# Kernel optimization log

Hardware: AMD Instinct MI355X
Metric: run time of the kernel (lower is better)

The kernel has to match this reference:

```python
import jax, jax.numpy as jnp
import numpy as np

DIM = 2048
K_DIM = 2048
Q_HEADS = 16
KV_HEADS = 4
HEAD_DIM = DIM // Q_HEADS  # 128
KV_DIM = HEAD_DIM * KV_HEADS  # 512
MAX_LEN = 2048
ROPE_THETA = 10000.0
ROPE_FACTOR = 8.0


def _rope_cos_sin(seq_len):
    # Faithful to generate_sin_cos_pos_emb with is_causal=True
    d = HEAD_DIM
    seq_eff = max(seq_len, MAX_LEN)
    base_adj = (ROPE_FACTOR * seq_eff / MAX_LEN - (ROPE_FACTOR - 1.0)) ** (d / (d - 2))
    adjusted_base = ROPE_THETA * base_adj
    inv_freq = 1.0 / adjusted_base ** (np.arange(0, d, 2, dtype=np.float32) / d)
    pos = np.arange(seq_len, dtype=np.float32)  # causal: no centering
    freqs = pos[:, None] * inv_freq[None, :]            # [S, d/2]
    emb = np.concatenate([freqs, freqs], axis=-1)        # [S, d]
    return jnp.asarray(np.cos(emb), jnp.float32), jnp.asarray(np.sin(emb), jnp.float32)


def _rotate_half(x):
    x1, x2 = jnp.split(x, 2, axis=-1)
    return jnp.concatenate([-x2, x1], axis=-1)


def setup_inputs() -> dict:
    key = jax.random.key(0)
    ks = jax.random.split(key, 12)
    B, S = 1, 2048
    s_in = 1.0 / np.sqrt(DIM)
    s_k = 1.0 / np.sqrt(K_DIM)
    return {
        "query": jax.random.normal(ks[0], (B, S, DIM), jnp.float32),
        "key": jax.random.normal(ks[1], (B, S, K_DIM), jnp.float32),
        "value": jax.random.normal(ks[2], (B, S, K_DIM), jnp.float32),
        "Wq": jax.random.uniform(ks[3], (DIM, DIM), jnp.float32, -s_in, s_in),
        "bq": jax.random.uniform(ks[4], (DIM,), jnp.float32, -s_in, s_in),
        "Wk": jax.random.uniform(ks[5], (KV_DIM, K_DIM), jnp.float32, -s_k, s_k),
        "bk": jax.random.uniform(ks[6], (KV_DIM,), jnp.float32, -s_k, s_k),
        "Wv": jax.random.uniform(ks[7], (KV_DIM, K_DIM), jnp.float32, -s_k, s_k),
        "bv": jax.random.uniform(ks[8], (KV_DIM,), jnp.float32, -s_k, s_k),
        "Wo": jax.random.uniform(ks[9], (DIM, DIM), jnp.float32, -s_in, s_in),
        "bo": jax.random.uniform(ks[10], (DIM,), jnp.float32, -s_in, s_in),
    }


def reference(query, key, value, Wq, bq, Wk, bk, Wv, bv, Wo, bo):
    B, S, _ = query.shape
    scale = HEAD_DIM ** -0.5

    q = query @ Wq.T + bq                                   # [B,S,DIM]
    k = key @ Wk.T + bk                                     # [B,S,KV_DIM]
    v = value @ Wv.T + bv                                   # [B,S,KV_DIM]

    q = q.reshape(B, S, Q_HEADS, HEAD_DIM)
    k = k.reshape(B, S, KV_HEADS, HEAD_DIM)
    v = v.reshape(B, S, KV_HEADS, HEAD_DIM)

    cos, sin = _rope_cos_sin(S)                              # [S,D]
    cos = cos[None, :, None, :]
    sin = sin[None, :, None, :]
    q = q * cos + _rotate_half(q) * sin
    k = k * cos + _rotate_half(k) * sin

    # [B,H,S,D]
    q = q.transpose(0, 2, 1, 3)
    k = k.transpose(0, 2, 1, 3)
    v = v.transpose(0, 2, 1, 3)

    rep = Q_HEADS // KV_HEADS
    k = jnp.repeat(k, rep, axis=1)
    v = jnp.repeat(v, rep, axis=1)

    scores = jnp.einsum('bhqd,bhkd->bhqk', q, k) * scale
    causal = jnp.tril(jnp.ones((S, S), bool))
    scores = jnp.where(causal[None, None], scores, jnp.finfo(scores.dtype).min)
    attn = jax.nn.softmax(scores, axis=-1)
    out = jnp.einsum('bhqk,bhkd->bhqd', attn, v)             # [B,H,S,D]

    out = out.transpose(0, 2, 1, 3).reshape(B, S, DIM)
    return out @ Wo.T + bo
```

## Files before the change

### kernel.cpp

```cpp
#include <hip/hip_runtime.h>
#include <stdint.h>

typedef __attribute__((ext_vector_type(8))) short short8;
typedef __attribute__((ext_vector_type(4))) float f32x4;
typedef __attribute__((ext_vector_type(4))) unsigned short u16x4;
typedef unsigned short bf16_t;

__device__ __forceinline__ bf16_t f2bf(float f) {
  union { float f; uint32_t u; } x; x.f = f;
  uint32_t r = x.u + 0x7fffu + ((x.u >> 16) & 1u);
  return (bf16_t)(r >> 16);
}

__device__ __forceinline__ void ld_g2l_16(const bf16_t* g, bf16_t* l) {
  __builtin_amdgcn_global_load_lds(
      (const __attribute__((address_space(1))) void*)g,
      (__attribute__((address_space(3))) void*)l, 16, 0, 0);
}

__global__ void convert_all(const float* __restrict__ s0, const float* __restrict__ s1,
                            const float* __restrict__ s2, const float* __restrict__ s3,
                            const float* __restrict__ s4, const float* __restrict__ s5,
                            const float* __restrict__ s6,
                            bf16_t* __restrict__ d0, bf16_t* __restrict__ d1,
                            bf16_t* __restrict__ d2, bf16_t* __restrict__ d3,
                            bf16_t* __restrict__ d4, bf16_t* __restrict__ d5,
                            bf16_t* __restrict__ d6,
                            float* __restrict__ CS, float* __restrict__ SN) {
  int i = blockIdx.x * 256 + threadIdx.x;
  if (i < 131072) {
    int fi = i & 63, pos = i >> 6;
    float ang = (float)pos * exp2f((float)fi * -0.2076205059f);
    CS[i] = cosf(ang);
    SN[i] = sinf(ang);
  }
  const float* src; bf16_t* dst; int off;
  if (i < 5 * 1048576) {
    int t = i >> 20; off = i & 1048575;
    if (t == 0)      { src = s0; dst = d0; }
    else if (t == 1) { src = s1; dst = d1; }
    else if (t == 2) { src = s2; dst = d2; }
    else if (t == 3) { src = s3; dst = d3; }
    else             { src = s4; dst = d4; }
  } else {
    int j = i - 5 * 1048576;
    if (j < 262144) { src = s5; dst = d5; off = j; }
    else            { src = s6; dst = d6; off = j - 262144; }
  }
  f32x4 v = *(const f32x4*)(src + (size_t)off * 4);
  u16x4 o;
  o[0] = f2bf(v[0]); o[1] = f2bf(v[1]); o[2] = f2bf(v[2]); o[3] = f2bf(v[3]);
  *(u16x4*)(dst + (size_t)off * 4) = o;
}

template <int MODE>
__device__ __forceinline__ void gemm_core(
    bf16_t* __restrict__ As, bf16_t* __restrict__ Bs,
    const bf16_t* __restrict__ A, const bf16_t* __restrict__ Bm,
    const float* __restrict__ bias, void* __restrict__ Cout,
    int N, int K, int m0, int n0,
    const float* __restrict__ CS, const float* __restrict__ SN) {
  const int tid = threadIdx.x;
  const int lane = tid & 63, quad = lane >> 4, l16 = lane & 15;
  const int wv = tid >> 6;
  const int wr = wv >> 1, wc = wv & 1;

  f32x4 acc[2][4];
  const f32x4 zf = {0.f, 0.f, 0.f, 0.f};
#pragma unroll
  for (int mi = 0; mi < 2; ++mi)
#pragma unroll
    for (int ni = 0; ni < 4; ++ni) acc[mi][ni] = zf;

  const int rA = tid >> 2, cA = (tid & 3) * 8;
  const bf16_t* Ap  = A + (size_t)(m0 + rA) * K + cA;
  const bf16_t* Bp0 = Bm + (size_t)(n0 + rA) * K + cA;
  const bf16_t* Bp1 = Bm + (size_t)(n0 + 64 + rA) * K + cA;

  auto STAGE = [&](int buf, int k0) {
    ld_g2l_16(Ap + k0, As + buf * 2048 + tid * 8);
    ld_g2l_16(Bp0 + k0, Bs + buf * 4096 + tid * 8);
    ld_g2l_16(Bp1 + k0, Bs + buf * 4096 + (tid + 256) * 8);
  };

  STAGE(0, 0);
  __syncthreads();
  int buf = 0;

  for (int k0 = 0; k0 < K; k0 += 32) {
    if (k0 + 32 < K) STAGE(buf ^ 1, k0 + 32);
    const bf16_t* Ab = As + buf * 2048;
    const bf16_t* Bb = Bs + buf * 4096;
    short8 af[2], bf[4];
#pragma unroll
    for (int mi = 0; mi < 2; ++mi)
      af[mi] = *(const short8*)(&Ab[(wr * 32 + mi * 16 + l16) * 32 + quad * 8]);
#pragma unroll
    for (int ni = 0; ni < 4; ++ni)
      bf[ni] = *(const short8*)(
          &Bb[(wc * 32 + (ni & 1) * 16 + (ni >> 1) * 64 + l16) * 32 + quad * 8]);
#pragma unroll
    for (int mi = 0; mi < 2; ++mi)
#pragma unroll
      for (int ni = 0; ni < 4; ++ni)
        acc[mi][ni] = __builtin_amdgcn_mfma_f32_16x16x32_bf16(
            af[mi], bf[ni], acc[mi][ni], 0, 0, 0);
    __asm__ volatile("s_waitcnt vmcnt(0)" ::: "memory");
    __syncthreads();
    buf ^= 1;
  }

  if (MODE == 0 || MODE == 2) {
#pragma unroll
    for (int mi = 0; mi < 2; ++mi)
#pragma unroll
      for (int ni = 0; ni < 4; ++ni) {
        int n = n0 + wc * 32 + (ni & 1) * 16 + (ni >> 1) * 64 + l16;
        int mbase = m0 + wr * 32 + mi * 16 + quad * 4;
        float bv = bias[n];
#pragma unroll
        for (int r = 0; r < 4; ++r) {
          float v = acc[mi][ni][r] + bv;
          int m = mbase + r;
          if (MODE == 0) ((float*)Cout)[(size_t)m * N + n] = v;
          else           ((bf16_t*)Cout)[(size_t)n * 2048 + m] = f2bf(v);
        }
      }
  } else {
    const float scale = (MODE == 3) ? 0.12751744f : 1.0f;
    bf16_t* dst = (bf16_t*)Cout;
#pragma unroll
    for (int mi = 0; mi < 2; ++mi)
#pragma unroll
      for (int r = 0; r < 4; ++r) {
        int m = m0 + wr * 32 + mi * 16 + quad * 4 + r;
#pragma unroll
        for (int ni = 0; ni < 2; ++ni) {
          int i = wc * 32 + ni * 16 + l16;
          int n_lo = n0 + i;
          float v1 = acc[mi][ni][r] + bias[n_lo];
          float v2 = acc[mi][ni + 2][r] + bias[n_lo + 64];
          float c = CS[m * 64 + i];
          float s = SN[m * 64 + i];
          float o1 = (v1 * c - v2 * s) * scale;
          float o2 = (v2 * c + v1 * s) * scale;
          dst[(size_t)m * N + n_lo] = f2bf(o1);
          dst[(size_t)m * N + n_lo + 64] = f2bf(o2);
        }
      }
  }
}

__global__ __launch_bounds__(256) void gemm_qkv(
    const bf16_t* __restrict__ qb, const bf16_t* __restrict__ kb,
    const bf16_t* __restrict__ vb, const bf16_t* __restrict__ wqb,
    const bf16_t* __restrict__ wkb, const bf16_t* __restrict__ wvb,
    const float* __restrict__ bq, const float* __restrict__ bk,
    const float* __restrict__ bv, bf16_t* __restrict__ Qr,
    bf16_t* __restrict__ Kr, bf16_t* __restrict__ Vt,
    const float* __restrict__ CS, const float* __restrict__ SN) {
  __shared__ __align__(16) bf16_t As[2 * 64 * 32];
  __shared__ __align__(16) bf16_t Bs[2 * 128 * 32];
  int bx = blockIdx.x, m0 = blockIdx.y * 64;
  if (bx < 16)
    gemm_core<3>(As, Bs, qb, wqb, bq, Qr, 2048, 2048, m0, bx * 128, CS, SN);
  else if (bx < 20)
    gemm_core<4>(As, Bs, kb, wkb, bk, Kr, 512, 2048, m0, (bx - 16) * 128, CS, SN);
  else
    gemm_core<2>(As, Bs, vb, wvb, bv, Vt, 512, 2048, m0, (bx - 20) * 128, CS, SN);
}

__global__ __launch_bounds__(256) void gemm_o(
    const bf16_t* __restrict__ Ob, const bf16_t* __restrict__ wob,
    const float* __restrict__ bo, float* __restrict__ out) {
  __shared__ __align__(16) bf16_t As[2 * 64 * 32];
  __shared__ __align__(16) bf16_t Bs[2 * 128 * 32];
  gemm_core<0>(As, Bs, Ob, wob, bo, out, 2048, 2048,
               blockIdx.y * 64, blockIdx.x * 128, nullptr, nullptr);
}

__global__ __launch_bounds__(256, 2) void attn_fwd(
    const bf16_t* __restrict__ Qr, const bf16_t* __restrict__ Kr,
    const bf16_t* __restrict__ Vt, bf16_t* __restrict__ Oo) {
  const int h = blockIdx.y;
  const int bx = blockIdx.x;
  const int qt = (h < 8) ? (31 - bx) : bx;
  const int T = qt + 1;

  const int tid = threadIdx.x;
  const int wv = tid >> 6, lane = tid & 63, quad = lane >> 4, l16 = lane & 15;
  const int q_base = qt * 64 + wv * 16;
  const int hkv = h >> 2;
  const int qg = q_base + l16;
  const int swzE = (l16 & 7) << 3;

  __shared__ __align__(16) bf16_t Ks[2][64 * 128];
  __shared__ __align__(16) bf16_t Vs[2][128 * 64];

  short8 qf[4];
  {
    const bf16_t* qp = Qr + (size_t)qg * 2048 + h * 128 + quad * 8;
#pragma unroll
    for (int kc = 0; kc < 4; ++kc) qf[kc] = *(const short8*)(qp + kc * 32);
  }

  const f32x4 zf = {0.f, 0.f, 0.f, 0.f};
  f32x4 o[8];
#pragma unroll
  for (int di = 0; di < 8; ++di) o[di] = zf;
  float l_acc = 0.f;

  auto STAGE = [&](int buf, int t) {
    const int k0 = t * 64;
    bf16_t* KB = &Ks[buf][0];
    bf16_t* VB = &Vs[buf][0];
#pragma unroll
    for (int m = 0; m < 4; ++m) {
      int rK = wv * 16 + m * 4 + (lane >> 4);
      const bf16_t* gK = Kr + (size_t)(k0 + rK) * 512 + hkv * 128
                         + (((lane & 15) ^ ((4 * (m & 1)) | quad)) << 3);
      ld_g2l_16(gK, KB + rK * 128 + ((lane & 15) << 3));
      int rV = wv * 32 + m * 8 + (lane >> 3);
      const bf16_t* gV = Vt + (size_t)(hkv * 128 + rV) * 2048 + k0
                         + (((lane & 7) ^ ((lane >> 3) & 7)) << 3);
      ld_g2l_16(gV, VB + rV * 64 + ((lane & 7) << 3));
    }
  };

  STAGE(0, 0);
  __syncthreads();
  int buf = 0;

  for (int t = 0; t < T; ++t) {
    if (t + 1 < T) STAGE(buf ^ 1, t + 1);
    const bf16_t* KB = &Ks[buf][0];
    const bf16_t* VB = &Vs[buf][0];
    const int k0 = t * 64;

    f32x4 sacc[4];
#pragma unroll
    for (int sub = 0; sub < 4; ++sub) sacc[sub] = zf;
#pragma unroll
    for (int sub = 0; sub < 4; ++sub)
#pragma unroll
      for (int kc = 0; kc < 4; ++kc) {
        short8 kf = *(const short8*)(
            &KB[(sub * 16 + l16) * 128 + ((kc * 32 + quad * 8) ^ swzE)]);
        sacc[sub] = __builtin_amdgcn_mfma_f32_16x16x32_bf16(kf, qf[kc], sacc[sub], 0, 0, 0);
      }

    const bool dg = (k0 + 63 > q_base);
    uint32_t Dw[4][2];
#pragma unroll
    for (int sub = 0; sub < 4; ++sub) {
      float pv[4];
#pragma unroll
      for (int r = 0; r < 4; ++r) {
        float e = exp2f(sacc[sub][r]);
        if (dg) {
          int kg = k0 + sub * 16 + quad * 4 + r;
          if (kg > qg) e = 0.f;
        }
        pv[r] = e;
        l_acc += e;
      }
      asm("v_cvt_pk_bf16_f32 %0, %1, %2" : "=v"(Dw[sub][0]) : "v"(pv[0]), "v"(pv[1]));
      asm("v_cvt_pk_bf16_f32 %0, %1, %2" : "=v"(Dw[sub][1]) : "v"(pv[2]), "v"(pv[3]));
    }

    const int aA = ((((quad * 2) & 3) << 4) + l16) << 2;
    const int aB = ((((quad * 2 + 1) & 3) << 4) + l16) << 2;
    const bool losel = quad < 2;
#define BPERM(a, x) ((uint32_t)__builtin_amdgcn_ds_bpermute((a), (int)(x)))
    union { uint32_t w[4]; short8 v; } U0, U1;
    {
      uint32_t t0, t1;
      t0 = BPERM(aA, Dw[0][0]); t1 = BPERM(aA, Dw[1][0]); U0.w[0] = losel ? t0 : t1;
      t0 = BPERM(aA, Dw[0][1]); t1 = BPERM(aA, Dw[1][1]); U0.w[1] = losel ? t0 : t1;
      t0 = BPERM(aB, Dw[0][0]); t1 = BPERM(aB, Dw[1][0]); U0.w[2] = losel ? t0 : t1;
      t0 = BPERM(aB, Dw[0][1]); t1 = BPERM(aB, Dw[1][1]); U0.w[3] = losel ? t0 : t1;
      t0 = BPERM(aA, Dw[2][0]); t1 = BPERM(aA, Dw[3][0]); U1.w[0] = losel ? t0 : t1;
      t0 = BPERM(aA, Dw[2][1]); t1 = BPERM(aA, Dw[3][1]); U1.w[1] = losel ? t0 : t1;
      t0 = BPERM(aB, Dw[2][0]); t1 = BPERM(aB, Dw[3][0]); U1.w[2] = losel ? t0 : t1;
      t0 = BPERM(aB, Dw[2][1]); t1 = BPERM(aB, Dw[3][1]); U1.w[3] = losel ? t0 : t1;
    }
#undef BPERM
    const short8 pf0 = U0.v, pf1 = U1.v;

#pragma unroll
    for (int di = 0; di < 8; ++di) {
      short8 vf0 = *(const short8*)(
          &VB[(di * 16 + l16) * 64 + ((quad * 8) ^ swzE)]);
      short8 vf1 = *(const short8*)(
          &VB[(di * 16 + l16) * 64 + ((quad * 8 + 32) ^ swzE)]);
      o[di] = __builtin_amdgcn_mfma_f32_16x16x32_bf16(pf0, vf0, o[di], 0, 0, 0);
      o[di] = __builtin_amdgcn_mfma_f32_16x16x32_bf16(pf1, vf1, o[di], 0, 0, 0);
    }

    __asm__ volatile("s_waitcnt vmcnt(0)" ::: "memory");
    __syncthreads();
    buf ^= 1;
  }

  float lf = l_acc;
  lf += __shfl_xor(lf, 16);
  lf += __shfl_xor(lf, 32);
  float linv[4];
#pragma unroll
  for (int r = 0; r < 4; ++r) linv[r] = 1.0f / __shfl(lf, quad * 4 + r, 64);
#pragma unroll
  for (int di = 0; di < 8; ++di)
#pragma unroll
    for (int r = 0; r < 4; ++r) {
      size_t row = q_base + quad * 4 + r;
      size_t col = h * 128 + di * 16 + l16;
      Oo[row * 2048 + col] = f2bf(o[di][r] * linv[r]);
    }
}

extern "C" void kernel_launch(void* const* d_in, const int* in_sizes, int n_in,
                              void* d_out, int out_size, void* d_ws, size_t ws_size,
                              hipStream_t stream) {
  (void)in_sizes; (void)n_in; (void)out_size; (void)ws_size;
  const float* query = (const float*)d_in[0];
  const float* key = (const float*)d_in[1];
  const float* value = (const float*)d_in[2];
  const float* Wq = (const float*)d_in[3];
  const float* bq = (const float*)d_in[4];
  const float* Wk = (const float*)d_in[5];
  const float* bk = (const float*)d_in[6];
  const float* Wv = (const float*)d_in[7];
  const float* bv = (const float*)d_in[8];
  const float* Wo = (const float*)d_in[9];
  const float* bo = (const float*)d_in[10];
  float* out = (float*)d_out;

  char* ws = (char*)d_ws;
  const size_t MB = 1024 * 1024;
  bf16_t* qb  = (bf16_t*)(ws + 0 * MB);
  bf16_t* kb  = (bf16_t*)(ws + 8 * MB);
  bf16_t* vb  = (bf16_t*)(ws + 16 * MB);
  bf16_t* wqb = (bf16_t*)(ws + 24 * MB);
  bf16_t* wkb = (bf16_t*)(ws + 32 * MB);
  bf16_t* wvb = (bf16_t*)(ws + 34 * MB);
  bf16_t* wob = (bf16_t*)(ws + 36 * MB);
  bf16_t* Qr  = (bf16_t*)(ws + 44 * MB);
  bf16_t* Kr  = (bf16_t*)(ws + 52 * MB);
  bf16_t* Vt  = (bf16_t*)(ws + 54 * MB);
  bf16_t* Ob  = (bf16_t*)(ws + 56 * MB);
  float*  CS  = (float*)(ws + 64 * MB);
  float*  SN  = (float*)(ws + 64 * MB + 512 * 1024);

  convert_all<<<22528, 256, 0, stream>>>(query, key, value, Wq, Wo, Wk, Wv,
                                         qb, kb, vb, wqb, wob, wkb, wvb, CS, SN);
  gemm_qkv<<<dim3(24, 32), 256, 0, stream>>>(qb, kb, vb, wqb, wkb, wvb,
                                             bq, bk, bv, Qr, Kr, Vt, CS, SN);
  attn_fwd<<<dim3(32, 16), 256, 0, stream>>>(Qr, Kr, Vt, Ob);
  gemm_o<<<dim3(16, 32), 256, 0, stream>>>(Ob, wob, bo, out);
}
```

Before: 276.8 us.

## Triple-buffer GEMM LDS staging with XOR swizzle and XCD-aware block remap

The shared GEMM core goes from double to triple buffering. It prefetches two K-steps ahead and waits with a partial vmcnt so global-to-LDS loads overlap more compute. An XOR swizzle is applied to the global source columns and the LDS fragment reads to reduce bank conflicts. Both GEMM launches become 1D grids whose block IDs are remapped so consecutive jobs land on the same XCD, aiming for better L2 reuse. The extra LDS buffer raises shared memory use per block.

```diff
diff --git a/kernel.cpp b/kernel.cpp
--- a/kernel.cpp
+++ b/kernel.cpp
@@ -64,6 +64,7 @@
   const int lane = tid & 63, quad = lane >> 4, l16 = lane & 15;
   const int wv = tid >> 6;
   const int wr = wv >> 1, wc = wv & 1;
+  const int swz = ((l16 >> 1) & 3) << 3;
 
   f32x4 acc[2][4];
   const f32x4 zf = {0.f, 0.f, 0.f, 0.f};
@@ -72,10 +73,11 @@
 #pragma unroll
     for (int ni = 0; ni < 4; ++ni) acc[mi][ni] = zf;
 
-  const int rA = tid >> 2, cA = (tid & 3) * 8;
-  const bf16_t* Ap  = A + (size_t)(m0 + rA) * K + cA;
-  const bf16_t* Bp0 = Bm + (size_t)(n0 + rA) * K + cA;
-  const bf16_t* Bp1 = Bm + (size_t)(n0 + 64 + rA) * K + cA;
+  const int rT = tid >> 2;
+  const int colsw = (((tid & 3) ^ ((tid >> 3) & 3)) << 3);
+  const bf16_t* Ap  = A + (size_t)(m0 + rT) * K + colsw;
+  const bf16_t* Bp0 = Bm + (size_t)(n0 + rT) * K + colsw;
+  const bf16_t* Bp1 = Bm + (size_t)(n0 + 64 + rT) * K + colsw;
 
   auto STAGE = [&](int buf, int k0) {
     ld_g2l_16(Ap + k0, As + buf * 2048 + tid * 8);
@@ -84,30 +86,39 @@
   };
 
   STAGE(0, 0);
-  __syncthreads();
-  int buf = 0;
-
+  STAGE(1, 32);
+  __asm__ volatile("s_waitcnt vmcnt(3)" ::: "memory");
+  __builtin_amdgcn_s_barrier();
+
+  int bcur = 0, bst = 2;
   for (int k0 = 0; k0 < K; k0 += 32) {
-    if (k0 + 32 < K) STAGE(buf ^ 1, k0 + 32);
-    const bf16_t* Ab = As + buf * 2048;
-    const bf16_t* Bb = Bs + buf * 4096;
-    short8 af[2], bf[4];
+    if (k0 + 64 < K) STAGE(bst, k0 + 64);
+    const bf16_t* Ab = As + bcur * 2048;
+    const bf16_t* Bb = Bs + bcur * 4096;
+    short8 af[2], bfv[4];
 #pragma unroll
     for (int mi = 0; mi < 2; ++mi)
-      af[mi] = *(const short8*)(&Ab[(wr * 32 + mi * 16 + l16) * 32 + quad * 8]);
+      af[mi] = *(const short8*)(
+          &Ab[(wr * 32 + mi * 16 + l16) * 32 + ((quad * 8) ^ swz)]);
 #pragma unroll
     for (int ni = 0; ni < 4; ++ni)
-      bf[ni] = *(const short8*)(
-          &Bb[(wc * 32 + (ni & 1) * 16 + (ni >> 1) * 64 + l16) * 32 + quad * 8]);
+      bfv[ni] = *(const short8*)(
+          &Bb[(wc * 32 + (ni & 1) * 16 + (ni >> 1) * 64 + l16) * 32 +
+              ((quad * 8) ^ swz)]);
 #pragma unroll
     for (int mi = 0; mi < 2; ++mi)
 #pragma unroll
       for (int ni = 0; ni < 4; ++ni)
         acc[mi][ni] = __builtin_amdgcn_mfma_f32_16x16x32_bf16(
-            af[mi], bf[ni], acc[mi][ni], 0, 0, 0);
-    __asm__ volatile("s_waitcnt vmcnt(0)" ::: "memory");
-    __syncthreads();
-    buf ^= 1;
+            af[mi], bfv[ni], acc[mi][ni], 0, 0, 0);
+    if (k0 + 64 < K) {
+      __asm__ volatile("s_waitcnt vmcnt(3)" ::: "memory");
+    } else {
+      __asm__ volatile("s_waitcnt vmcnt(0)" ::: "memory");
+    }
+    __builtin_amdgcn_s_barrier();
+    bcur = (bcur == 2) ? 0 : bcur + 1;
+    bst  = (bst == 2) ? 0 : bst + 1;
   }
 
   if (MODE == 0 || MODE == 2) {
@@ -159,9 +170,11 @@
     const float* __restrict__ bv, bf16_t* __restrict__ Qr,
     bf16_t* __restrict__ Kr, bf16_t* __restrict__ Vt,
     const float* __restrict__ CS, const float* __restrict__ SN) {
-  __shared__ __align__(16) bf16_t As[2 * 64 * 32];
-  __shared__ __align__(16) bf16_t Bs[2 * 128 * 32];
-  int bx = blockIdx.x, m0 = blockIdx.y * 64;
+  __shared__ __align__(16) bf16_t As[3 * 64 * 32];
+  __shared__ __align__(16) bf16_t Bs[3 * 128 * 32];
+  int bid = blockIdx.x;
+  int job = (bid & 7) * 96 + (bid >> 3);
+  int bx = job >> 5, m0 = (job & 31) * 64;
   if (bx < 16)
     gemm_core<3>(As, Bs, qb, wqb, bq, Qr, 2048, 2048, m0, bx * 128, CS, SN);
   else if (bx < 20)
@@ -173,10 +186,13 @@
 __global__ __launch_bounds__(256) void gemm_o(
     const bf16_t* __restrict__ Ob, const bf16_t* __restrict__ wob,
     const float* __restrict__ bo, float* __restrict__ out) {
-  __shared__ __align__(16) bf16_t As[2 * 64 * 32];
-  __shared__ __align__(16) bf16_t Bs[2 * 128 * 32];
-  gemm_core<0>(As, Bs, Ob, wob, bo, out, 2048, 2048,
-               blockIdx.y * 64, blockIdx.x * 128, nullptr, nullptr);
+  __shared__ __align__(16) bf16_t As[3 * 64 * 32];
+  __shared__ __align__(16) bf16_t Bs[3 * 128 * 32];
+  int bid = blockIdx.x;
+  int job = (bid & 7) * 64 + (bid >> 3);
+  int bx = job >> 5, m0 = (job & 31) * 64;
+  gemm_core<0>(As, Bs, Ob, wob, bo, out, 2048, 2048, m0, bx * 128,
+               nullptr, nullptr);
 }
 
 __global__ __launch_bounds__(256, 2) void attn_fwd(
@@ -353,8 +369,8 @@
 
   convert_all<<<22528, 256, 0, stream>>>(query, key, value, Wq, Wo, Wk, Wv,
                                          qb, kb, vb, wqb, wob, wkb, wvb, CS, SN);
-  gemm_qkv<<<dim3(24, 32), 256, 0, stream>>>(qb, kb, vb, wqb, wkb, wvb,
-                                             bq, bk, bv, Qr, Kr, Vt, CS, SN);
+  gemm_qkv<<<768, 256, 0, stream>>>(qb, kb, vb, wqb, wkb, wvb,
+                                    bq, bk, bv, Qr, Kr, Vt, CS, SN);
   attn_fwd<<<dim3(32, 16), 256, 0, stream>>>(Qr, Kr, Vt, Ob);
-  gemm_o<<<dim3(16, 32), 256, 0, stream>>>(Ob, wob, bo, out);
-}
+  gemm_o<<<512, 256, 0, stream>>>(Ob, wob, bo, out);
+}
```

After: 273.4 us. Within noise of the previous version (-1.2%).
